# Optimization experiments

Hardware: AMD Instinct MI355X
Metric: run time of the kernel (lower is better)

## Reference

```python
import jax, jax.numpy as jnp
import numpy as np

D_MODEL = 512; N_HEADS = 8; D_HEAD = 64; N_LAYERS = 4; D_FF = 2048
B = 4; L_PROJ = 4096; L_IMG = 4096
EPS_ATTN = 1e-6; EPS_LN = 1e-5


def _ln_params(*lead):
    gb = jnp.stack([jnp.ones(D_MODEL, jnp.float32), jnp.zeros(D_MODEL, jnp.float32)])  # [2, d] (gamma, beta)
    return jnp.broadcast_to(gb, lead + (2, D_MODEL))


def setup_inputs() -> dict:
    key = jax.random.key(0)
    ks = jax.random.split(key, 16)
    s = 0.02
    d, f, L = D_MODEL, D_FF, N_LAYERS
    rn = lambda i, shape: jax.random.normal(ks[i], shape, jnp.float32)
    return {
        'x': rn(0, (B, L_PROJ, 2)),
        'out_pos_emb': rn(1, (1, L_IMG, d)),
        'pe_input': rn(2, (L_PROJ, d // 2)),
        'emb_w': rn(3, (2, d // 2)) * s, 'emb_b': jnp.zeros((d // 2,), jnp.float32),
        'enc_attn_w': rn(4, (L, 4, d, d)) * s, 'enc_attn_b': jnp.zeros((L, 4, d), jnp.float32),
        'enc_ln': _ln_params(L, 2),
        'enc_ff_w1': rn(5, (L, d, f)) * s, 'enc_ff_b1': jnp.zeros((L, f), jnp.float32),
        'enc_ff_w2': rn(6, (L, f, d)) * s, 'enc_ff_b2': jnp.zeros((L, d), jnp.float32),
        'enc_final_ln': _ln_params(),
        'dec_self_w': rn(7, (L, 4, d, d)) * s, 'dec_self_b': jnp.zeros((L, 4, d), jnp.float32),
        'dec_cross_w': rn(8, (L, 4, d, d)) * s, 'dec_cross_b': jnp.zeros((L, 4, d), jnp.float32),
        'dec_ln': _ln_params(L, 3),
        'dec_ff_w1': rn(9, (L, d, f)) * s, 'dec_ff_b1': jnp.zeros((L, f), jnp.float32),
        'dec_ff_w2': rn(10, (L, f, d)) * s, 'dec_ff_b2': jnp.zeros((L, d), jnp.float32),
        'dec_final_ln': _ln_params(),
        'pred_w': rn(11, (d, 2)) * s, 'pred_b': jnp.zeros((2,), jnp.float32),
    }


def layer_norm(x, gb):
    mu = jnp.mean(x, -1, keepdims=True)
    xc = x - mu
    var = jnp.mean(xc * xc, -1, keepdims=True)
    return xc * jax.lax.rsqrt(var + EPS_LN) * gb[0] + gb[1]


def linear_attention(q, k, v):
    # q:[b,l,h,d] k,v:[b,s,h,d]; feature map phi(x)=elu(x)+1 (fast_transformers LinearAttention)
    Q = jax.nn.elu(q) + 1.0
    K = jax.nn.elu(k) + 1.0
    kv = jnp.einsum('bshd,bshm->bhdm', K, v)                      # [b,h,d,d]
    z = 1.0 / (jnp.einsum('blhd,bhd->blh', Q, jnp.sum(K, axis=1)) + EPS_ATTN)
    return jnp.einsum('blhd,bhdm,blh->blhm', Q, kv, z)


def attention(xq, xkv, w, b):
    # fast_transformers AttentionLayer: project, split heads, linear attn, merge, out-project
    Bq, Lq, d = xq.shape
    Lk = xkv.shape[1]
    q = (xq @ w[0] + b[0]).reshape(Bq, Lq, N_HEADS, D_HEAD)
    k = (xkv @ w[1] + b[1]).reshape(Bq, Lk, N_HEADS, D_HEAD)
    v = (xkv @ w[2] + b[2]).reshape(Bq, Lk, N_HEADS, D_HEAD)
    o = linear_attention(q, k, v).reshape(Bq, Lq, d)
    return o @ w[3] + b[3]


def ffn(x, w1, b1, w2, b2):
    return jax.nn.relu(x @ w1 + b1) @ w2 + b2


def reference(x, out_pos_emb, pe_input, emb_w, emb_b,
              enc_attn_w, enc_attn_b, enc_ln, enc_ff_w1, enc_ff_b1, enc_ff_w2, enc_ff_b2, enc_final_ln,
              dec_self_w, dec_self_b, dec_cross_w, dec_cross_b, dec_ln, dec_ff_w1, dec_ff_b1, dec_ff_w2, dec_ff_b2, dec_final_ln,
              pred_w, pred_b):
    Bq = x.shape[0]
    # Fourier coefficient embedding + concatenated 2D positional encoding
    h = x @ emb_w + emb_b                                         # [B,Lp,d/2]
    pe = jnp.broadcast_to(pe_input[None], (Bq,) + pe_input.shape)
    h = jnp.concatenate([h, pe], axis=-1)                          # [B,Lp,d]
    # Encoder (fast_transformers post-norm layer order)
    for l in range(N_LAYERS):
        h = h + attention(h, h, enc_attn_w[l], enc_attn_b[l])
        h = layer_norm(h, enc_ln[l, 0])
        y = ffn(h, enc_ff_w1[l], enc_ff_b1[l], enc_ff_w2[l], enc_ff_b2[l])
        h = layer_norm(h + y, enc_ln[l, 1])
    z = layer_norm(h, enc_final_ln)
    # Decoder queries: target pos embedding tiled over batch (repeat_interleave dim=0)
    o = jnp.repeat(out_pos_emb, Bq, axis=0)                        # [B,Li,d]
    for l in range(N_LAYERS):
        o = o + attention(o, o, dec_self_w[l], dec_self_b[l])
        o = layer_norm(o, dec_ln[l, 0])
        o = o + attention(o, z, dec_cross_w[l], dec_cross_b[l])
        o = layer_norm(o, dec_ln[l, 1])
        y = ffn(o, dec_ff_w1[l], dec_ff_b1[l], dec_ff_w2[l], dec_ff_b2[l])
        o = layer_norm(o + y, dec_ln[l, 2])
    o = layer_norm(o, dec_final_ln)
    return o @ pred_w + pred_b                                     # [B,Li,2]
```

## Files before the change

### kernel.cpp

```cpp
#include <hip/hip_runtime.h>
#include <cstddef>

#define B_  4
#define L_  4096
#define D_  512
#define H_  8
#define DH_ 64
#define F_  2048
#define M_  (B_*L_)
#define NLAYERS 4
#define EPS_LN   1e-5f
#define EPS_ATTN 1e-6f

#define EPI_NONE 0
#define EPI_RELU 1
#define EPI_PHI  2

typedef unsigned short ushort_t;
typedef short short8 __attribute__((ext_vector_type(8)));
typedef float float4v __attribute__((ext_vector_type(4)));

__device__ inline ushort_t f2bf(float f) {
    union { float f; unsigned u; } c; c.f = f;
    unsigned u = c.u;
    unsigned r = (u + 0x7fffu + ((u >> 16) & 1u)) >> 16;
    return (ushort_t)r;
}
__device__ inline float bf2f(ushort_t h) {
    union { unsigned u; float f; } c; c.u = ((unsigned)h) << 16;
    return c.f;
}

__device__ inline void async16(const ushort_t* g, ushort_t* lds) {
    __builtin_amdgcn_global_load_lds(
        (const __attribute__((address_space(1))) unsigned int*)g,
        (__attribute__((address_space(3))) unsigned int*)lds, 16, 0, 0);
}

__device__ inline void swz(int& bx, int& by) {
    int gx = gridDim.x, gy = gridDim.y;
    int b = blockIdx.y * gx + blockIdx.x;
    int xcd = b & 7;
    int slot = b >> 3;
    bx = slot % gx;
    by = xcd * (gy >> 3) + slot / gx;
}

__global__ __launch_bounds__(256, 2) void mfma_gemm(
    const ushort_t* __restrict__ A, const ushort_t* __restrict__ Wt,
    const float* __restrict__ bias, const float* __restrict__ resid,
    float* __restrict__ Cf, ushort_t* __restrict__ Cb,
    int N, int K, int epi)
{
    __shared__ ushort_t As[2][128 * 32];
    __shared__ ushort_t Bs[2][128 * 32];

    int bxi, byi;
    swz(bxi, byi);
    const int bm = byi * 128;
    const int bn = bxi * 128;
    const int tid = threadIdx.x;
    const int w = tid >> 6;
    const int lane = tid & 63;
    const int wm = w >> 1, wn = w & 1;
    const int quad = lane >> 4;
    const int m16 = lane & 15;
    const int rsub = lane >> 2;
    const int c8 = (lane & 3) * 8;

    auto stage = [&](int k0, int bid) {
        #pragma unroll
        for (int i = 0; i < 2; ++i) {
            async16(A  + (size_t)(bm + i*64 + w*16 + rsub) * K + k0 + c8,
                    &As[bid][i*2048 + w*512]);
            async16(Wt + (size_t)(bn + i*64 + w*16 + rsub) * K + k0 + c8,
                    &Bs[bid][i*2048 + w*512]);
        }
    };

    float4v acc[4][4];
    #pragma unroll
    for (int i = 0; i < 4; ++i)
        #pragma unroll
        for (int j = 0; j < 4; ++j)
            acc[i][j] = (float4v){0.f, 0.f, 0.f, 0.f};

    const int nIter = K >> 5;
    stage(0, 0);
    for (int it = 0; it < nIter; ++it) {
        __syncthreads();
        if (it + 1 < nIter) stage((it + 1) << 5, (it + 1) & 1);
        const ushort_t* as = As[it & 1];
        const ushort_t* bs = Bs[it & 1];

        short8 af[4], bf[4];
        #pragma unroll
        for (int i = 0; i < 4; ++i) {
            af[i] = *(const short8*)&as[(wm*64 + i*16 + m16) * 32 + quad*8];
            bf[i] = *(const short8*)&bs[(wn*64 + i*16 + m16) * 32 + quad*8];
        }
        #pragma unroll
        for (int i = 0; i < 4; ++i)
            #pragma unroll
            for (int j = 0; j < 4; ++j)
                acc[i][j] = __builtin_amdgcn_mfma_f32_16x16x32_bf16(
                    af[i], bf[j], acc[i][j], 0, 0, 0);
    }

    #pragma unroll
    for (int i = 0; i < 4; ++i) {
        #pragma unroll
        for (int j = 0; j < 4; ++j) {
            #pragma unroll
            for (int r = 0; r < 4; ++r) {
                int m = bm + wm*64 + i*16 + quad*4 + r;
                int n = bn + wn*64 + j*16 + m16;
                float v = acc[i][j][r] + bias[n];
                if (resid) v += resid[(size_t)m * N + n];
                if (epi == EPI_RELU)     v = fmaxf(v, 0.f);
                else if (epi == EPI_PHI) v = (v > 0.f) ? (v + 1.f) : __expf(v);
                if (Cf) Cf[(size_t)m * N + n] = v;
                if (Cb) Cb[(size_t)m * N + n] = f2bf(v);
            }
        }
    }
}

__global__ __launch_bounds__(256, 2) void gemm_kv(
    const ushort_t* __restrict__ A, const ushort_t* __restrict__ Wt,
    const float* __restrict__ bias, int nq,
    ushort_t* __restrict__ Qb,
    ushort_t* __restrict__ Kt, ushort_t* __restrict__ Vt)
{
    const int K = 512;
    __shared__ ushort_t As[2][128 * 32];
    __shared__ ushort_t Bs[2][128 * 32];

    int bxi, byi;
    swz(bxi, byi);
    const int bm = byi * 128;
    const int bn = bxi * 128;
    const int tid = threadIdx.x;
    const int w = tid >> 6;
    const int lane = tid & 63;
    const int wm = w >> 1, wn = w & 1;
    const int quad = lane >> 4;
    const int m16 = lane & 15;
    const int rsub = lane >> 2;
    const int c8 = (lane & 3) * 8;

    auto stage = [&](int k0, int bid) {
        #pragma unroll
        for (int i = 0; i < 2; ++i) {
            async16(A  + (size_t)(bm + i*64 + w*16 + rsub) * K + k0 + c8,
                    &As[bid][i*2048 + w*512]);
            async16(Wt + (size_t)(bn + i*64 + w*16 + rsub) * K + k0 + c8,
                    &Bs[bid][i*2048 + w*512]);
        }
    };

    float4v acc[4][4];
    #pragma unroll
    for (int i = 0; i < 4; ++i)
        #pragma unroll
        for (int j = 0; j < 4; ++j)
            acc[i][j] = (float4v){0.f, 0.f, 0.f, 0.f};

    const int nIter = K >> 5;
    stage(0, 0);
    for (int it = 0; it < nIter; ++it) {
        __syncthreads();
        if (it + 1 < nIter) stage((it + 1) << 5, (it + 1) & 1);
        const ushort_t* as = As[it & 1];
        const ushort_t* bs = Bs[it & 1];
        short8 af[4], bf[4];
        #pragma unroll
        for (int i = 0; i < 4; ++i) {
            af[i] = *(const short8*)&as[(wm*64 + i*16 + m16) * 32 + quad*8];
            bf[i] = *(const short8*)&bs[(wn*64 + i*16 + m16) * 32 + quad*8];
        }
        #pragma unroll
        for (int i = 0; i < 4; ++i)
            #pragma unroll
            for (int j = 0; j < 4; ++j)
                acc[i][j] = __builtin_amdgcn_mfma_f32_16x16x32_bf16(
                    af[i], bf[j], acc[i][j], 0, 0, 0);
    }

    #pragma unroll
    for (int i = 0; i < 4; ++i) {
        int m0 = bm + wm*64 + i*16 + quad*4;
        int b  = m0 >> 12;
        int l  = m0 & (L_ - 1);
        #pragma unroll
        for (int j = 0; j < 4; ++j) {
            int n = bn + wn*64 + j*16 + m16;
            if (n < nq) {
                #pragma unroll
                for (int r = 0; r < 4; ++r) {
                    float v = acc[i][j][r] + bias[n];
                    v = (v > 0.f) ? (v + 1.f) : __expf(v);
                    Qb[(size_t)(m0 + r) * D_ + n] = f2bf(v);
                }
            } else {
                int nk = n - nq;
                bool isK = nk < 512;
                int nn = isK ? nk : nk - 512;
                int h = nn >> 6, dd = nn & 63;
                union { ushort_t u[4]; uint2 v2; } pk;
                #pragma unroll
                for (int r = 0; r < 4; ++r) {
                    float v = acc[i][j][r] + bias[n];
                    if (isK) v = (v > 0.f) ? (v + 1.f) : __expf(v);
                    pk.u[r] = f2bf(v);
                }
                ushort_t* dst = isK
                    ? Kt + ((size_t)(b*H_ + h) * 64 + dd) * L_ + l
                    : Vt + ((size_t)(b*H_ + h) * 64 + dd) * L_ + l;
                *(uint2*)dst = pk.v2;
            }
        }
    }
}

__global__ __launch_bounds__(256) void kv_mfma(const ushort_t* __restrict__ Kt,
                                               const ushort_t* __restrict__ Vt,
                                               float* __restrict__ kvp)
{
    __shared__ ushort_t Ks[2][64 * 32];
    __shared__ ushort_t Vs[2][64 * 32];

    const int bh = blockIdx.x;
    const int sc = blockIdx.y;
    const int CS = L_ / 8;
    const ushort_t* Kg = Kt + (size_t)bh * 64 * L_;
    const ushort_t* Vg = Vt + (size_t)bh * 64 * L_;

    const int tid = threadIdx.x;
    const int w = tid >> 6;
    const int lane = tid & 63;
    const int quad = lane >> 4;
    const int m16 = lane & 15;
    const int rsub = lane >> 2;
    const int c8 = (lane & 3) * 8;

    auto stage = [&](int s0, int bid) {
        async16(Kg + (size_t)(w*16 + rsub) * L_ + s0 + c8, &Ks[bid][w*512]);
        async16(Vg + (size_t)(w*16 + rsub) * L_ + s0 + c8, &Vs[bid][w*512]);
    };

    short8 onesfrag;
    {
        ushort_t v = (m16 == 0) ? (ushort_t)0x3F80 : (ushort_t)0;
        #pragma unroll
        for (int j = 0; j < 8; ++j) onesfrag[j] = (short)v;
    }

    float4v acc[5];
    #pragma unroll
    for (int i = 0; i < 5; ++i) acc[i] = (float4v){0.f, 0.f, 0.f, 0.f};

    const int sbase = sc * CS;
    const int nIter = CS >> 5;
    stage(sbase, 0);
    for (int it = 0; it < nIter; ++it) {
        __syncthreads();
        if (it + 1 < nIter) stage(sbase + ((it + 1) << 5), (it + 1) & 1);
        const ushort_t* ks = Ks[it & 1];
        const ushort_t* vs = Vs[it & 1];

        short8 bfrag = *(const short8*)&ks[(w*16 + m16) * 32 + quad*8];
        #pragma unroll
        for (int nt = 0; nt < 4; ++nt) {
            short8 afrag = *(const short8*)&vs[(nt*16 + m16) * 32 + quad*8];
            acc[nt] = __builtin_amdgcn_mfma_f32_16x16x32_bf16(
                afrag, bfrag, acc[nt], 0, 0, 0);
        }
        acc[4] = __builtin_amdgcn_mfma_f32_16x16x32_bf16(
            onesfrag, bfrag, acc[4], 0, 0, 0);
    }

    float* dst = kvp + ((size_t)sc * 32 + bh) * 80 * 64;
    #pragma unroll
    for (int nt = 0; nt < 5; ++nt)
        #pragma unroll
        for (int r = 0; r < 4; ++r) {
            int n = nt*16 + quad*4 + r;
            int d = w*16 + m16;
            dst[n * 64 + d] = acc[nt][r];
        }
}

__global__ void kv_reduce(const float* __restrict__ kvp, ushort_t* __restrict__ kvb)
{
    int i = blockIdx.x * 256 + threadIdx.x;
    float s = 0.f;
    #pragma unroll
    for (int sc = 0; sc < 8; ++sc)
        s += kvp[(size_t)sc * 32 * 80 * 64 + i];
    kvb[i] = f2bf(s);
}

__global__ __launch_bounds__(256) void attn_out_mfma(const ushort_t* __restrict__ Q,
                                                     const ushort_t* __restrict__ kvb,
                                                     ushort_t* __restrict__ ab)
{
    __shared__ ushort_t Qs[128 * 64];
    __shared__ float zbuf[128];

    const int bh = blockIdx.x;
    const int h = bh & 7, b = bh >> 3;
    const int l0 = blockIdx.y * 128;

    const int tid = threadIdx.x;
    const int w = tid >> 6;
    const int lane = tid & 63;
    const int quad = lane >> 4;
    const int m16 = lane & 15;

    const ushort_t* kv = kvb + (size_t)bh * 80 * 64;
    short8 bf[5][2];
    #pragma unroll
    for (int j = 0; j < 5; ++j)
        #pragma unroll
        for (int t = 0; t < 2; ++t)
            bf[j][t] = *(const short8*)(kv + (j*16 + m16) * 64 + t*32 + quad*8);

    #pragma unroll
    for (int i = 0; i < 4; ++i)
        async16(Q + (size_t)(b*L_ + l0 + i*32 + w*8 + (lane >> 3)) * D_
                  + h*64 + (lane & 7)*8,
                &Qs[(i*32 + w*8) * 64]);
    __syncthreads();

    float4v acc[2][5];
    #pragma unroll
    for (int i = 0; i < 2; ++i)
        #pragma unroll
        for (int j = 0; j < 5; ++j)
            acc[i][j] = (float4v){0.f, 0.f, 0.f, 0.f};

    #pragma unroll
    for (int t = 0; t < 2; ++t) {
        short8 af[2];
        #pragma unroll
        for (int i = 0; i < 2; ++i)
            af[i] = *(const short8*)&Qs[(w*32 + i*16 + m16) * 64 + t*32 + quad*8];
        #pragma unroll
        for (int i = 0; i < 2; ++i)
            #pragma unroll
            for (int j = 0; j < 5; ++j)
                acc[i][j] = __builtin_amdgcn_mfma_f32_16x16x32_bf16(
                    af[i], bf[j][t], acc[i][j], 0, 0, 0);
    }

    if (m16 == 0) {
        #pragma unroll
        for (int i = 0; i < 2; ++i)
            #pragma unroll
            for (int r = 0; r < 4; ++r)
                zbuf[w*32 + i*16 + quad*4 + r] = acc[i][4][r];
    }
    __syncthreads();

    #pragma unroll
    for (int i = 0; i < 2; ++i) {
        #pragma unroll
        for (int r = 0; r < 4; ++r) {
            int lrow = w*32 + i*16 + quad*4 + r;
            float zin = 1.f / (zbuf[lrow] + EPS_ATTN);
            #pragma unroll
            for (int j = 0; j < 4; ++j) {
                ab[(size_t)(b*L_ + l0 + lrow) * D_ + h*64 + j*16 + m16]
                    = f2bf(acc[i][j][r] * zin);
            }
        }
    }
}

__global__ __launch_bounds__(256) void wconv_kernel(const float* __restrict__ src,
                                                    ushort_t* __restrict__ dst,
                                                    int K, int N)
{
    __shared__ float tile[32][33];
    size_t moff = (size_t)blockIdx.z * K * N;
    src += moff; dst += moff;
    int n0 = blockIdx.x * 32, k0 = blockIdx.y * 32;
    int tx = threadIdx.x & 31, ty = threadIdx.x >> 5;
    #pragma unroll
    for (int i = 0; i < 4; ++i)
        tile[ty + i*8][tx] = src[(size_t)(k0 + ty + i*8) * N + n0 + tx];
    __syncthreads();
    #pragma unroll
    for (int i = 0; i < 4; ++i)
        dst[(size_t)(n0 + ty + i*8) * K + k0 + tx] = f2bf(tile[tx][ty + i*8]);
}

__global__ void embed_kernel(const float* __restrict__ x, const float* __restrict__ pe,
                             const float* __restrict__ ew, const float* __restrict__ eb,
                             float* __restrict__ hf, ushort_t* __restrict__ hb)
{
    size_t row = blockIdx.x;
    int c = threadIdx.x;
    int l = (int)(row % L_);
    float x0 = x[row*2], x1 = x[row*2+1];
    float v0 = fmaf(x0, ew[c], fmaf(x1, ew[256 + c], eb[c]));
    float v1 = pe[(size_t)l*256 + c];
    hf[row*(size_t)D_ + c]       = v0;
    hf[row*(size_t)D_ + 256 + c] = v1;
    hb[row*(size_t)D_ + c]       = f2bf(v0);
    hb[row*(size_t)D_ + 256 + c] = f2bf(v1);
}

__global__ void bcast_kernel(const float* __restrict__ src,
                             float* __restrict__ dstf, ushort_t* __restrict__ dstb)
{
    size_t i = (size_t)blockIdx.x * 256 + threadIdx.x;
    float v = src[i];
    ushort_t bb16 = f2bf(v);
    #pragma unroll
    for (int bb = 0; bb < B_; ++bb) {
        dstf[(size_t)bb * L_ * D_ + i] = v;
        dstb[(size_t)bb * L_ * D_ + i] = bb16;
    }
}

__global__ __launch_bounds__(256) void ln_kernel(const float* __restrict__ X,
                                                 const float* __restrict__ gb,
                                                 float* __restrict__ Yf,
                                                 ushort_t* __restrict__ Yb)
{
    int row = blockIdx.x * 4 + (threadIdx.x >> 6);
    int lane = threadIdx.x & 63;
    const float* x = X + (size_t)row * D_;
    float v[8];
    float s = 0.f;
    #pragma unroll
    for (int i = 0; i < 8; ++i) { v[i] = x[lane + i*64]; s += v[i]; }
    #pragma unroll
    for (int off = 32; off >= 1; off >>= 1) s += __shfl_xor(s, off, 64);
    float mu = s * (1.f / D_);
    float sq = 0.f;
    #pragma unroll
    for (int i = 0; i < 8; ++i) { float d = v[i] - mu; sq += d * d; }
    #pragma unroll
    for (int off = 32; off >= 1; off >>= 1) sq += __shfl_xor(sq, off, 64);
    float rstd = rsqrtf(sq * (1.f / D_) + EPS_LN);
    #pragma unroll
    for (int i = 0; i < 8; ++i) {
        int c = lane + i*64;
        float y = (v[i] - mu) * rstd * gb[c] + gb[512 + c];
        Yf[(size_t)row * D_ + c] = y;
        if (Yb) Yb[(size_t)row * D_ + c] = f2bf(y);
    }
}

__global__ __launch_bounds__(256) void pred_kernel(const float* __restrict__ X,
                                                   const float* __restrict__ pw,
                                                   const float* __restrict__ pb,
                                                   float* __restrict__ out)
{
    int row = blockIdx.x * 4 + (threadIdx.x >> 6);
    int lane = threadIdx.x & 63;
    const float* x = X + (size_t)row * D_;
    float a0 = 0.f, a1 = 0.f;
    #pragma unroll
    for (int i = 0; i < 8; ++i) {
        int c = lane + i*64;
        float v = x[c];
        a0 = fmaf(v, pw[c*2 + 0], a0);
        a1 = fmaf(v, pw[c*2 + 1], a1);
    }
    #pragma unroll
    for (int off = 32; off >= 1; off >>= 1) {
        a0 += __shfl_xor(a0, off, 64);
        a1 += __shfl_xor(a1, off, 64);
    }
    if (lane == 0) {
        out[(size_t)row*2 + 0] = a0 + pb[0];
        out[(size_t)row*2 + 1] = a1 + pb[1];
    }
}

extern "C" void kernel_launch(void* const* d_in, const int* in_sizes, int n_in,
                              void* d_out, int out_size, void* d_ws, size_t ws_size,
                              hipStream_t stream)
{
    const float* x            = (const float*)d_in[0];
    const float* out_pos_emb  = (const float*)d_in[1];
    const float* pe_input     = (const float*)d_in[2];
    const float* emb_w        = (const float*)d_in[3];
    const float* emb_b        = (const float*)d_in[4];
    const float* enc_attn_w   = (const float*)d_in[5];
    const float* enc_attn_b   = (const float*)d_in[6];
    const float* enc_ln       = (const float*)d_in[7];
    const float* enc_ff_w1    = (const float*)d_in[8];
    const float* enc_ff_b1    = (const float*)d_in[9];
    const float* enc_ff_w2    = (const float*)d_in[10];
    const float* enc_ff_b2    = (const float*)d_in[11];
    const float* enc_final_ln = (const float*)d_in[12];
    const float* dec_self_w   = (const float*)d_in[13];
    const float* dec_self_b   = (const float*)d_in[14];
    const float* dec_cross_w  = (const float*)d_in[15];
    const float* dec_cross_b  = (const float*)d_in[16];
    const float* dec_ln       = (const float*)d_in[17];
    const float* dec_ff_w1    = (const float*)d_in[18];
    const float* dec_ff_b1    = (const float*)d_in[19];
    const float* dec_ff_w2    = (const float*)d_in[20];
    const float* dec_ff_b2    = (const float*)d_in[21];
    const float* dec_final_ln = (const float*)d_in[22];
    const float* pred_w       = (const float*)d_in[23];
    const float* pred_b       = (const float*)d_in[24];
    float* out = (float*)d_out;

    const size_t MD = (size_t)M_ * D_;
    float*    h_f32 = (float*)d_ws;
    ushort_t* h_b   = (ushort_t*)(h_f32 + MD);
    ushort_t* z_b   = h_b + MD;
    ushort_t* un    = z_b + MD;
    ushort_t* Qb = un;
    ushort_t* ab = un + MD;
    ushort_t* Kt = un + 2*MD;
    ushort_t* Vt = un + 3*MD;
    ushort_t* ffh = un;
    const size_t UN_ELEMS = 4*MD;
    ushort_t* kvb = un + UN_ELEMS;
    float*    kvp = (float*)(kvb + (size_t)32*80*64);
    ushort_t* wts = (ushort_t*)(kvp + (size_t)8*32*80*64);

    const size_t ATT_MAT = (size_t)D_ * D_;
    const size_t ATT_LYR = 4 * ATT_MAT;
    const size_t FF_MAT  = (size_t)D_ * F_;
    ushort_t* wt_enc_att   = wts;
    ushort_t* wt_dec_self  = wt_enc_att  + 4 * ATT_LYR;
    ushort_t* wt_dec_cross = wt_dec_self + 4 * ATT_LYR;
    ushort_t* wt_enc_ff1   = wt_dec_cross + 4 * ATT_LYR;
    ushort_t* wt_enc_ff2   = wt_enc_ff1  + 4 * FF_MAT;
    ushort_t* wt_dec_ff1   = wt_enc_ff2  + 4 * FF_MAT;
    ushort_t* wt_dec_ff2   = wt_dec_ff1  + 4 * FF_MAT;

    hipLaunchKernelGGL(wconv_kernel, dim3(16, 16, 16), dim3(256), 0, stream,
                       enc_attn_w, wt_enc_att, D_, D_);
    hipLaunchKernelGGL(wconv_kernel, dim3(16, 16, 16), dim3(256), 0, stream,
                       dec_self_w, wt_dec_self, D_, D_);
    hipLaunchKernelGGL(wconv_kernel, dim3(16, 16, 16), dim3(256), 0, stream,
                       dec_cross_w, wt_dec_cross, D_, D_);
    hipLaunchKernelGGL(wconv_kernel, dim3(64, 16, 4), dim3(256), 0, stream,
                       enc_ff_w1, wt_enc_ff1, D_, F_);
    hipLaunchKernelGGL(wconv_kernel, dim3(16, 64, 4), dim3(256), 0, stream,
                       enc_ff_w2, wt_enc_ff2, F_, D_);
    hipLaunchKernelGGL(wconv_kernel, dim3(64, 16, 4), dim3(256), 0, stream,
                       dec_ff_w1, wt_dec_ff1, D_, F_);
    hipLaunchKernelGGL(wconv_kernel, dim3(16, 64, 4), dim3(256), 0, stream,
                       dec_ff_w2, wt_dec_ff2, F_, D_);

    auto gemm = [&](const ushort_t* A, const ushort_t* Wt, const float* bias,
                    const float* resid, float* Cf, ushort_t* Cb, int N, int K, int epi) {
        dim3 grid(N / 128, M_ / 128);
        hipLaunchKernelGGL(mfma_gemm, grid, dim3(256), 0, stream,
                           A, Wt, bias, resid, Cf, Cb, N, K, epi);
    };
    auto layernorm = [&](const float* gb, ushort_t* Yb) {
        hipLaunchKernelGGL(ln_kernel, dim3(M_ / 4), dim3(256), 0, stream,
                           h_f32, gb, h_f32, Yb);
    };
    auto attn = [&](const ushort_t* xq_b, const ushort_t* xkv_b, bool self,
                    const ushort_t* wt, const float* bv) {
        if (self) {
            hipLaunchKernelGGL(gemm_kv, dim3(12, 128), dim3(256), 0, stream,
                               xkv_b, wt, bv, 512, Qb, Kt, Vt);
        } else {
            gemm(xq_b, wt, bv, nullptr, nullptr, Qb, D_, D_, EPI_PHI);
            hipLaunchKernelGGL(gemm_kv, dim3(8, 128), dim3(256), 0, stream,
                               xkv_b, wt + ATT_MAT, bv + D_, 0, nullptr, Kt, Vt);
        }
        hipLaunchKernelGGL(kv_mfma, dim3(32, 8), dim3(256), 0, stream, Kt, Vt, kvp);
        hipLaunchKernelGGL(kv_reduce, dim3(32*80*64/256), dim3(256), 0, stream,
                           kvp, kvb);
        hipLaunchKernelGGL(attn_out_mfma, dim3(32, 32), dim3(256), 0, stream,
                           Qb, kvb, ab);
        gemm(ab, wt + 3*ATT_MAT, bv + 3*D_, h_f32, h_f32, nullptr, D_, D_, EPI_NONE);
    };
    auto ffn = [&](const ushort_t* wt1, const float* b1,
                   const ushort_t* wt2, const float* b2) {
        gemm(h_b, wt1, b1, nullptr, nullptr, ffh, F_, D_, EPI_RELU);
        gemm(ffh, wt2, b2, h_f32, h_f32, nullptr, D_, F_, EPI_NONE);
    };

    hipLaunchKernelGGL(embed_kernel, dim3(M_), dim3(256), 0, stream,
                       x, pe_input, emb_w, emb_b, h_f32, h_b);

    for (int l = 0; l < NLAYERS; ++l) {
        attn(h_b, h_b, true, wt_enc_att + l * ATT_LYR, enc_attn_b + (size_t)l * 4 * D_);
        layernorm(enc_ln + (size_t)(l*2 + 0) * 2 * D_, h_b);
        ffn(wt_enc_ff1 + l * FF_MAT, enc_ff_b1 + (size_t)l * F_,
            wt_enc_ff2 + l * FF_MAT, enc_ff_b2 + (size_t)l * D_);
        layernorm(enc_ln + (size_t)(l*2 + 1) * 2 * D_, h_b);
    }
    layernorm(enc_final_ln, z_b);

    hipLaunchKernelGGL(bcast_kernel, dim3(L_ * D_ / 256), dim3(256), 0, stream,
                       out_pos_emb, h_f32, h_b);
    for (int l = 0; l < NLAYERS; ++l) {
        attn(h_b, h_b, true, wt_dec_self + l * ATT_LYR, dec_self_b + (size_t)l * 4 * D_);
        layernorm(dec_ln + (size_t)(l*3 + 0) * 2 * D_, h_b);
        attn(h_b, z_b, false, wt_dec_cross + l * ATT_LYR, dec_cross_b + (size_t)l * 4 * D_);
        layernorm(dec_ln + (size_t)(l*3 + 1) * 2 * D_, h_b);
        ffn(wt_dec_ff1 + l * FF_MAT, dec_ff_b1 + (size_t)l * F_,
            wt_dec_ff2 + l * FF_MAT, dec_ff_b2 + (size_t)l * D_);
        layernorm(dec_ln + (size_t)(l*3 + 2) * 2 * D_, h_b);
    }
    layernorm(dec_final_ln, nullptr);

    hipLaunchKernelGGL(pred_kernel, dim3(M_ / 4), dim3(256), 0, stream,
                       h_f32, pred_w, pred_b, out);
}
```

Before: 2.881 ms.

## Triple-buffer LDS staging in GEMM and KV kernels with vmcnt-based waits

Moves the mfma_gemm, gemm_kv and kv_mfma kernels from double to triple LDS buffering. Loads are issued two iterations ahead, and each step waits only for the oldest batch of async global-to-LDS loads via s_waitcnt vmcnt plus a raw barrier, replacing a full __syncthreads. The aim is to hide more global load latency behind MFMA work. In exchange, LDS use per block rises from 32KB to 48KB in the GEMMs, which may cut occupancy. Correctness also depends on the vmcnt counts exactly matching the number of loads issued per stage.

```diff
diff --git a/kernel.cpp b/kernel.cpp
--- a/kernel.cpp
+++ b/kernel.cpp
@@ -37,6 +37,9 @@
         (__attribute__((address_space(3))) unsigned int*)lds, 16, 0, 0);
 }
 
+#define WAIT_VM(n) __builtin_amdgcn_s_waitcnt(0x0F70 | (n))
+#define BARRIER_RAW() __builtin_amdgcn_s_barrier()
+
 __device__ inline void swz(int& bx, int& by) {
     int gx = gridDim.x, gy = gridDim.y;
     int b = blockIdx.y * gx + blockIdx.x;
@@ -52,8 +55,8 @@
     float* __restrict__ Cf, ushort_t* __restrict__ Cb,
     int N, int K, int epi)
 {
-    __shared__ ushort_t As[2][128 * 32];
-    __shared__ ushort_t Bs[2][128 * 32];
+    __shared__ ushort_t As[3][128 * 32];
+    __shared__ ushort_t Bs[3][128 * 32];
 
     int bxi, byi;
     swz(bxi, byi);
@@ -68,7 +71,8 @@
     const int rsub = lane >> 2;
     const int c8 = (lane & 3) * 8;
 
-    auto stage = [&](int k0, int bid) {
+    auto stage = [&](int it) {
+        int k0 = it << 5, bid = it % 3;
         #pragma unroll
         for (int i = 0; i < 2; ++i) {
             async16(A  + (size_t)(bm + i*64 + w*16 + rsub) * K + k0 + c8,
@@ -85,14 +89,9 @@
         for (int j = 0; j < 4; ++j)
             acc[i][j] = (float4v){0.f, 0.f, 0.f, 0.f};
 
-    const int nIter = K >> 5;
-    stage(0, 0);
-    for (int it = 0; it < nIter; ++it) {
-        __syncthreads();
-        if (it + 1 < nIter) stage((it + 1) << 5, (it + 1) & 1);
-        const ushort_t* as = As[it & 1];
-        const ushort_t* bs = Bs[it & 1];
-
+    auto compute = [&](int it) {
+        const ushort_t* as = As[it % 3];
+        const ushort_t* bs = Bs[it % 3];
         short8 af[4], bf[4];
         #pragma unroll
         for (int i = 0; i < 4; ++i) {
@@ -105,7 +104,20 @@
             for (int j = 0; j < 4; ++j)
                 acc[i][j] = __builtin_amdgcn_mfma_f32_16x16x32_bf16(
                     af[i], bf[j], acc[i][j], 0, 0, 0);
-    }
+    };
+
+    const int nIter = K >> 5;
+    stage(0);
+    if (nIter > 1) stage(1);
+    for (int it = 0; it < nIter - 1; ++it) {
+        WAIT_VM(4);
+        BARRIER_RAW();
+        if (it + 2 < nIter) stage(it + 2);
+        compute(it);
+    }
+    WAIT_VM(0);
+    BARRIER_RAW();
+    compute(nIter - 1);
 
     #pragma unroll
     for (int i = 0; i < 4; ++i) {
@@ -133,8 +145,8 @@
     ushort_t* __restrict__ Kt, ushort_t* __restrict__ Vt)
 {
     const int K = 512;
-    __shared__ ushort_t As[2][128 * 32];
-    __shared__ ushort_t Bs[2][128 * 32];
+    __shared__ ushort_t As[3][128 * 32];
+    __shared__ ushort_t Bs[3][128 * 32];
 
     int bxi, byi;
     swz(bxi, byi);
@@ -149,7 +161,8 @@
     const int rsub = lane >> 2;
     const int c8 = (lane & 3) * 8;
 
-    auto stage = [&](int k0, int bid) {
+    auto stage = [&](int it) {
+        int k0 = it << 5, bid = it % 3;
         #pragma unroll
         for (int i = 0; i < 2; ++i) {
             async16(A  + (size_t)(bm + i*64 + w*16 + rsub) * K + k0 + c8,
@@ -166,13 +179,9 @@
         for (int j = 0; j < 4; ++j)
             acc[i][j] = (float4v){0.f, 0.f, 0.f, 0.f};
 
-    const int nIter = K >> 5;
-    stage(0, 0);
-    for (int it = 0; it < nIter; ++it) {
-        __syncthreads();
-        if (it + 1 < nIter) stage((it + 1) << 5, (it + 1) & 1);
-        const ushort_t* as = As[it & 1];
-        const ushort_t* bs = Bs[it & 1];
+    auto compute = [&](int it) {
+        const ushort_t* as = As[it % 3];
+        const ushort_t* bs = Bs[it % 3];
         short8 af[4], bf[4];
         #pragma unroll
         for (int i = 0; i < 4; ++i) {
@@ -185,7 +194,19 @@
             for (int j = 0; j < 4; ++j)
                 acc[i][j] = __builtin_amdgcn_mfma_f32_16x16x32_bf16(
                     af[i], bf[j], acc[i][j], 0, 0, 0);
-    }
+    };
+
+    const int nIter = K >> 5;
+    stage(0); stage(1);
+    for (int it = 0; it < nIter - 1; ++it) {
+        WAIT_VM(4);
+        BARRIER_RAW();
+        if (it + 2 < nIter) stage(it + 2);
+        compute(it);
+    }
+    WAIT_VM(0);
+    BARRIER_RAW();
+    compute(nIter - 1);
 
     #pragma unroll
     for (int i = 0; i < 4; ++i) {
@@ -227,8 +248,8 @@
                                                const ushort_t* __restrict__ Vt,
                                                float* __restrict__ kvp)
 {
-    __shared__ ushort_t Ks[2][64 * 32];
-    __shared__ ushort_t Vs[2][64 * 32];
+    __shared__ ushort_t Ks[3][64 * 32];
+    __shared__ ushort_t Vs[3][64 * 32];
 
     const int bh = blockIdx.x;
     const int sc = blockIdx.y;
@@ -243,8 +264,10 @@
     const int m16 = lane & 15;
     const int rsub = lane >> 2;
     const int c8 = (lane & 3) * 8;
-
-    auto stage = [&](int s0, int bid) {
+    const int sbase = sc * CS;
+
+    auto stage = [&](int it) {
+        int s0 = sbase + (it << 5), bid = it % 3;
         async16(Kg + (size_t)(w*16 + rsub) * L_ + s0 + c8, &Ks[bid][w*512]);
         async16(Vg + (size_t)(w*16 + rsub) * L_ + s0 + c8, &Vs[bid][w*512]);
     };
@@ -260,15 +283,9 @@
     #pragma unroll
     for (int i = 0; i < 5; ++i) acc[i] = (float4v){0.f, 0.f, 0.f, 0.f};
 
-    const int sbase = sc * CS;
-    const int nIter = CS >> 5;
-    stage(sbase, 0);
-    for (int it = 0; it < nIter; ++it) {
-        __syncthreads();
-        if (it + 1 < nIter) stage(sbase + ((it + 1) << 5), (it + 1) & 1);
-        const ushort_t* ks = Ks[it & 1];
-        const ushort_t* vs = Vs[it & 1];
-
+    auto compute = [&](int it) {
+        const ushort_t* ks = Ks[it % 3];
+        const ushort_t* vs = Vs[it % 3];
         short8 bfrag = *(const short8*)&ks[(w*16 + m16) * 32 + quad*8];
         #pragma unroll
         for (int nt = 0; nt < 4; ++nt) {
@@ -278,7 +295,19 @@
         }
         acc[4] = __builtin_amdgcn_mfma_f32_16x16x32_bf16(
             onesfrag, bfrag, acc[4], 0, 0, 0);
-    }
+    };
+
+    const int nIter = CS >> 5;
+    stage(0); stage(1);
+    for (int it = 0; it < nIter - 1; ++it) {
+        WAIT_VM(2);
+        BARRIER_RAW();
+        if (it + 2 < nIter) stage(it + 2);
+        compute(it);
+    }
+    WAIT_VM(0);
+    BARRIER_RAW();
+    compute(nIter - 1);
 
     float* dst = kvp + ((size_t)sc * 32 + bh) * 80 * 64;
     #pragma unroll
```

New measurement: 2.932 ms. About the same (+1.8%).
